# Performance work log

Measured on AMD Instinct MI355X. Metric: run time of the kernel, lower is better.

Reference implementation:

```python
import jax, jax.numpy as jnp
import numpy as np

EPS = 1e-5
DN = ('NCHW', 'OIHW', 'NCHW')

def conv(x, w, b, stride, pad):
    y = jax.lax.conv_general_dilated(x, w, (stride, stride), [(pad, pad), (pad, pad)], dimension_numbers=DN)
    return y + b[None, :, None, None]

def instance_norm(x, gamma, beta):
    # normalize over spatial dims per (N, C)
    mu = jnp.mean(x, axis=(2, 3), keepdims=True)
    var = jnp.var(x, axis=(2, 3), keepdims=True)
    xh = (x - mu) * jax.lax.rsqrt(var + EPS)
    return xh * gamma[None, :, None, None] + beta[None, :, None, None]

def lrelu(x):
    return jnp.where(x >= 0, x, 0.2 * x)

def block(x, w, b, g, be, stride, pad):
    return lrelu(instance_norm(conv(x, w, b, stride, pad), g, be))

def setup_inputs() -> dict:
    key = jax.random.key(0)
    ks = jax.random.split(key, 16)
    dim = 64
    def rn(k, shape, s=0.05):
        return jax.random.normal(k, shape, dtype=jnp.float32) * s
    inp = {
        'x':   jax.random.normal(ks[0], (256, 3, 64, 64), dtype=jnp.float32),
        'w1': rn(ks[1], (dim, 3, 5, 5)),        'b1': jnp.zeros((dim,), jnp.float32),
        'g1': jnp.ones((dim,), jnp.float32),    'be1': jnp.zeros((dim,), jnp.float32),
        'w2': rn(ks[2], (dim*2, dim, 5, 5)),    'b2': jnp.zeros((dim*2,), jnp.float32),
        'g2': jnp.ones((dim*2,), jnp.float32),  'be2': jnp.zeros((dim*2,), jnp.float32),
        'w3': rn(ks[3], (dim*4, dim*2, 5, 5)),  'b3': jnp.zeros((dim*4,), jnp.float32),
        'g3': jnp.ones((dim*4,), jnp.float32),  'be3': jnp.zeros((dim*4,), jnp.float32),
        'w4': rn(ks[4], (dim*4, dim*4, 3, 3)),  'b4': jnp.zeros((dim*4,), jnp.float32),
        'g4': jnp.ones((dim*4,), jnp.float32),  'be4': jnp.zeros((dim*4,), jnp.float32),
        # MBD tensor T: (in_features=4096, out_features=64, kernel_dims=50), init N(0,1)
        'T':  jax.random.normal(ks[5], (4096, 64, 50), dtype=jnp.float32),
        'fc_w': rn(ks[6], (1000, 4096 + 64), s=0.02),
        'fc_b': jnp.zeros((1000,), jnp.float32),
    }
    return inp

def reference(x, w1, b1, g1, be1, w2, b2, g2, be2, w3, b3, g3, be3, w4, b4, g4, be4, T, fc_w, fc_b):
    bs = x.shape[0]
    f = block(x, w1, b1, g1, be1, 2, 2)   # (bs,64,32,32)
    f = block(f, w2, b2, g2, be2, 2, 2)   # (bs,128,16,16)
    f = block(f, w3, b3, g3, be3, 2, 2)   # (bs,256,8,8)
    f = block(f, w4, b4, g4, be4, 2, 1)   # (bs,256,4,4)
    feat = f.reshape(bs, -1)              # (bs,4096)
    # minibatch discrimination
    M = jnp.einsum('bi,iok->bok', feat, T)          # (bs,64,50)
    norm = jnp.sum(jnp.abs(M[None] - M[:, None]), axis=3)  # (bs,bs,64); [i,j]=|M_i-M_j|
    o_b = jnp.sum(jnp.exp(-norm), axis=0) - 1.0     # (bs,64)
    mb = jnp.concatenate([feat, o_b], axis=1)       # (bs,4160)
    y = mb @ fc_w.T + fc_b                          # (bs,1000)
    return feat, y
```

## Files before the change

### kernel.cpp

```cpp
#include <hip/hip_runtime.h>
#include <hip/hip_fp16.h>
#include <math.h>

#define EPSF 1e-5f

typedef __attribute__((ext_vector_type(4))) float  floatx4;
typedef __attribute__((ext_vector_type(4))) short  short4v;
typedef __attribute__((ext_vector_type(8))) short  short8v;

__device__ __forceinline__ unsigned short cvt_bf16(float f){
  unsigned u = __float_as_uint(f);
  unsigned r = (u + 0x7FFFu + ((u >> 16) & 1u)) >> 16;
  return (unsigned short)r;
}
__device__ __forceinline__ float bf2f(unsigned short h){
  return __uint_as_float(((unsigned)h) << 16);
}
__device__ __forceinline__ short8v ld_frag(const unsigned short* p){
  short4v lo = *(const short4v*)p;
  short4v hi = *(const short4v*)(p + 4);
  return __builtin_shufflevector(lo, hi, 0,1,2,3,4,5,6,7);
}
__device__ __forceinline__ float lrelu(float x){ return x >= 0.f ? x : 0.2f*x; }

__global__ __launch_bounds__(256) void prep_k(const float* __restrict__ w1, const float* __restrict__ w2,
                                              const float* __restrict__ w3, const float* __restrict__ w4,
                                              unsigned short* __restrict__ wb1, unsigned short* __restrict__ wb2,
                                              unsigned short* __restrict__ wb3, unsigned short* __restrict__ wb4,
                                              float* __restrict__ SQ){
  int b = blockIdx.x, t = threadIdx.x;
  if (b < 32){
    int idx = b*256 + t;
    int j = idx&7, lane = (idx>>3)&63, ks = (idx>>9)&3, grp = idx>>11;
    int co = grp*16 + (lane&15);
    int k = ks*32 + ((lane>>4)<<3) + j;
    int tap6 = k>>2, ci = k&3;
    int kh = tap6/6, kw = tap6 - kh*6;
    float v = 0.f;
    if (ci < 3 && kh < 5 && kw < 5) v = w1[(co*3 + ci)*25 + kh*5 + kw];
    wb1[idx] = cvt_bf16(v);
  } else if (b < 832){
    int idx = (b-32)*256 + t;
    int grp = idx/25600, rem = idx - grp*25600;
    int tap = rem/1024, rem2 = rem - tap*1024;
    int ccg = rem2>>9, lane = (rem2>>3)&63, j = rem2&7;
    int co = grp*16 + (lane&15);
    int ci = ccg*32 + ((lane>>4)<<3) + j;
    wb2[idx] = cvt_bf16(w2[(co*64 + ci)*25 + tap]);
  } else if (b < 4032){
    int idx = (b-832)*256 + t;
    int grp = idx/51200, rem = idx - grp*51200;
    int tap = rem/2048, rem2 = rem - tap*2048;
    int ccg = rem2>>9, lane = (rem2>>3)&63, j = rem2&7;
    int co = grp*16 + (lane&15);
    int ci = ccg*32 + ((lane>>4)<<3) + j;
    wb3[idx] = cvt_bf16(w3[(co*128 + ci)*25 + tap]);
  } else if (b < 6336){
    int idx = (b-4032)*256 + t;
    int grp = idx/36864, rem = idx - grp*36864;
    int tap = rem/4096, rem2 = rem - tap*4096;
    int ccg = rem2>>9, lane = (rem2>>3)&63, j = rem2&7;
    int co = grp*16 + (lane&15);
    int ci = ccg*32 + ((lane>>4)<<3) + j;
    wb4[idx] = cvt_bf16(w4[(co*256 + ci)*9 + tap]);
  } else {
    int idx = (b-6336)*256 + t;
    SQ[idx] = 0.f;
  }
}

__global__ __launch_bounds__(256) void packT_k(const float* __restrict__ T,
                                               unsigned short* __restrict__ Tp){
  const int b = blockIdx.x, t = threadIdx.x;
  __shared__ float tile[32][133];
  const int nb = b % 25, kt = b / 25;
  const int n0 = nb*128, k0 = kt*32;
  #pragma unroll
  for (int m=0;m<4;m++){
    int idx = m*256 + t;
    int row = idx>>5, c4 = (idx&31)<<2;
    const float4 v = *(const float4*)&T[(k0+row)*3200 + n0 + c4];
    tile[row][c4]   = v.x; tile[row][c4+1] = v.y;
    tile[row][c4+2] = v.z; tile[row][c4+3] = v.w;
  }
  __syncthreads();
  #pragma unroll
  for (int m=0;m<2;m++){
    int c = m*256 + t;
    int ngl = c>>6, lane = c&63, q = lane>>4, r = lane&15;
    unsigned short h[8];
    #pragma unroll
    for (int j=0;j<8;j++) h[j] = cvt_bf16(tile[q*8+j][ngl*16 + r]);
    *(uint4*)&Tp[(((nb*8 + ngl)*128 + kt)*64 + lane)*8] = *(const uint4*)h;
  }
}

__global__ __launch_bounds__(256) void packW_k(const float* __restrict__ W,
                                               unsigned short* __restrict__ Wp){
  int idx = blockIdx.x*256 + threadIdx.x;
  int lane = idx & 63, rem = idx >> 6;
  int kt = rem % 130, ng = rem / 130;
  int q = lane>>4, r = lane&15;
  int orow = ng*16 + r, k = kt*32 + (q<<3);
  unsigned short h[8] = {0,0,0,0,0,0,0,0};
  if (orow < 1000){
    float4 v0 = *(const float4*)&W[orow*4160 + k];
    float4 v1 = *(const float4*)&W[orow*4160 + k + 4];
    h[0]=cvt_bf16(v0.x); h[1]=cvt_bf16(v0.y); h[2]=cvt_bf16(v0.z); h[3]=cvt_bf16(v0.w);
    h[4]=cvt_bf16(v1.x); h[5]=cvt_bf16(v1.y); h[6]=cvt_bf16(v1.z); h[7]=cvt_bf16(v1.w);
  }
  *(uint4*)&Wp[idx*8] = *(const uint4*)h;
}

__global__ __launch_bounds__(256) void conv1_k(const float* __restrict__ x, const unsigned short* __restrict__ wb1P,
                                               float* __restrict__ S1, float* __restrict__ Q1,
                                               unsigned short* __restrict__ f1raw){
  const int t = threadIdx.x, n = blockIdx.x>>1, half = blockIdx.x&1;
  const int w = t>>6, lane = t&63, q = lane>>4, l16 = lane&15;
  __shared__ __align__(16) unsigned short img[36*68*4];
  short8v bf[4][4];
  #pragma unroll
  for (int nt=0;nt<4;nt++)
    #pragma unroll
    for (int ks=0;ks<4;ks++)
      bf[nt][ks] = *(const short8v*)&wb1P[((nt*4+ks)*64 + lane)*8];
  for (int i=t; i<4896; i+=256) ((unsigned*)img)[i] = 0u;
  __syncthreads();
  for (int idx=t; idx<1680; idx+=256){
    int ci = idx/560, rem = idx - ci*560;
    int tih = rem>>4, iw4 = (rem&15)<<2;
    int ih = half*32 - 2 + tih;
    if ((unsigned)ih < 64u){
      float4 v = *(const float4*)&x[((n*3+ci)<<12) + (ih<<6) + iw4];
      int base = (tih*68 + iw4 + 2)*4 + ci;
      img[base]    = cvt_bf16(v.x);
      img[base+4]  = cvt_bf16(v.y);
      img[base+8]  = cvt_bf16(v.z);
      img[base+12] = cvt_bf16(v.w);
    }
  }
  __syncthreads();
  floatx4 acc[8][4];
  #pragma unroll
  for (int mi=0;mi<8;mi++)
    #pragma unroll
    for (int nt=0;nt<4;nt++) acc[mi][nt] = (floatx4){0.f,0.f,0.f,0.f};
  #pragma unroll
  for (int mi=0; mi<8; mi++){
    int r = w*8 + mi;
    int ohl = r>>1, ow = ((r&1)<<4) + l16;
    #pragma unroll
    for (int ks=0; ks<4; ks++){
      int t0 = ks*8 + 2*q;
      int kh = t0/6, kw = t0 - kh*6;
      short8v a = ld_frag(&img[((ohl*2+kh)*68 + ow*2 + kw)*4]);
      #pragma unroll
      for (int nt=0; nt<4; nt++)
        acc[mi][nt] = __builtin_amdgcn_mfma_f32_16x16x32_bf16(a, bf[nt][ks], acc[mi][nt], 0,0,0);
    }
  }
  float sreg[4] = {0,0,0,0}, qreg[4] = {0,0,0,0};
  #pragma unroll
  for (int mi=0;mi<8;mi++){
    int r = w*8 + mi;
    #pragma unroll
    for (int nt=0;nt<4;nt++)
      #pragma unroll
      for (int e=0;e<4;e++){
        float v = acc[mi][nt][e];
        sreg[nt] += v; qreg[nt] += v*v;
        int px = half*512 + (r<<4) + (q<<2) + e;
        f1raw[(((n<<10)+px)<<6) + (nt<<4) + l16] = cvt_bf16(v);
      }
  }
  #pragma unroll
  for (int nt=0;nt<4;nt++){
    float s = sreg[nt], qq = qreg[nt];
    s  += __shfl_xor(s,16,64);  s  += __shfl_xor(s,32,64);
    qq += __shfl_xor(qq,16,64); qq += __shfl_xor(qq,32,64);
    if (q==0){
      atomicAdd(&S1[(n<<6) + (nt<<4) + l16], s);
      atomicAdd(&Q1[(n<<6) + (nt<<4) + l16], qq);
    }
  }
}

__global__ __launch_bounds__(512) void conv2_k(const unsigned short* __restrict__ fin,
                                               const unsigned short* __restrict__ wbP,
                                               const float* __restrict__ S1, const float* __restrict__ Q1,
                                               const float* __restrict__ g1, const float* __restrict__ be1,
                                               float* __restrict__ S2, float* __restrict__ Q2,
                                               unsigned short* __restrict__ fout){
  const int t = threadIdx.x;
  const int n = blockIdx.x >> 1, half = blockIdx.x & 1;
  const int w = t>>6, lane = t&63, q = lane>>4, l16 = lane&15;
  const int rw = w&1, cw = w>>1;
  __shared__ __align__(16) unsigned short tile[684*40];
  __shared__ float gmA[64], btA[64];
  if (t < 64){
    float S = S1[(n<<6)+t], Q = Q1[(n<<6)+t];
    float mu = S*(1.f/1024.f), var = fmaxf(Q*(1.f/1024.f) - mu*mu, 0.f);
    float r = rsqrtf(var+EPSF)*g1[t];
    gmA[t] = r; btA[t] = be1[t] - mu*r;
  }
  __syncthreads();
  floatx4 acc[4][2];
  #pragma unroll
  for (int mt=0;mt<4;mt++)
    #pragma unroll
    for (int nt=0;nt<2;nt++) acc[mt][nt] = (floatx4){0.f,0.f,0.f,0.f};
  int cellb[4];
  #pragma unroll
  for (int mt=0;mt<4;mt++){
    int r = rw*64 + mt*16 + l16;
    int ohl = r>>4, ow = r&15;
    cellb[mt] = (2*ohl)*36 + 2*ow;
  }
  for (int ccg = 0; ccg < 2; ccg++){
    const int cc = ccg<<5;
    if (ccg) __syncthreads();
    #pragma unroll
    for (int it=0; it<6; it++){
      int idx = it*512 + t;
      if (idx < 2736){
        int cell = idx>>2, ci0 = (idx&3)<<3;
        int tih = cell/36, tiw = cell - tih*36;
        int ih = half*16 + tih - 2, iw = tiw - 2;
        uint4 v = {0u,0u,0u,0u};
        if ((unsigned)ih < 32u && (unsigned)iw < 32u){
          v = *(const uint4*)&fin[(((n*32+ih)*32 + iw)<<6) + cc + ci0];
          unsigned short* hp = (unsigned short*)&v;
          #pragma unroll
          for (int jj=0;jj<8;jj++){
            int c = cc + ci0 + jj;
            hp[jj] = cvt_bf16(lrelu(bf2f(hp[jj])*gmA[c]+btA[c]));
          }
        }
        *(uint4*)&tile[cell*40 + ci0] = v;
      }
    }
    __syncthreads();
    const unsigned short* bp[2];
    #pragma unroll
    for (int nt=0;nt<2;nt++)
      bp[nt] = wbP + ((((cw*2+nt)*25)*2 + ccg)<<9) + lane*8;
    short8v bq[2][4];
    #pragma unroll
    for (int p=0;p<4;p++)
      #pragma unroll
      for (int nt=0;nt<2;nt++) bq[nt][p] = *(const short8v*)(bp[nt] + (p<<10));
    #pragma unroll
    for (int tap=0; tap<25; tap++){
      const int kh = tap/5, kw = tap - kh*5;
      const int aoff = kh*36 + kw;
      short8v a[4];
      #pragma unroll
      for (int mt=0;mt<4;mt++) a[mt] = *(const short8v*)&tile[(cellb[mt]+aoff)*40 + q*8];
      #pragma unroll
      for (int mt=0;mt<4;mt++)
        #pragma unroll
        for (int nt=0;nt<2;nt++)
          acc[mt][nt] = __builtin_amdgcn_mfma_f32_16x16x32_bf16(a[mt], bq[nt][tap&3], acc[mt][nt], 0,0,0);
      if (tap+4 < 25){
        #pragma unroll
        for (int nt=0;nt<2;nt++) bq[nt][tap&3] = *(const short8v*)(bp[nt] + ((tap+4)<<10));
      }
    }
  }
  #pragma unroll
  for (int nt=0;nt<2;nt++){
    int co = cw*32 + nt*16 + l16;
    float s=0.f, qq=0.f;
    #pragma unroll
    for (int mt=0;mt<4;mt++)
      #pragma unroll
      for (int e=0;e<4;e++){ float xv = acc[mt][nt][e]; s += xv; qq += xv*xv; }
    s  += __shfl_xor(s,16,64);  s  += __shfl_xor(s,32,64);
    qq += __shfl_xor(qq,16,64); qq += __shfl_xor(qq,32,64);
    if (q == 0){
      atomicAdd(&S2[n*128 + co], s);
      atomicAdd(&Q2[n*128 + co], qq);
    }
    #pragma unroll
    for (int mt=0;mt<4;mt++)
      #pragma unroll
      for (int e=0;e<4;e++){
        int px = half*128 + rw*64 + mt*16 + q*4 + e;
        fout[((n<<8) + px)*128 + co] = cvt_bf16(acc[mt][nt][e]);
      }
  }
}

__global__ __launch_bounds__(512) void conv3_k(const unsigned short* __restrict__ fin,
                                               const unsigned short* __restrict__ wbP,
                                               const float* __restrict__ S2, const float* __restrict__ Q2,
                                               const float* __restrict__ g2, const float* __restrict__ be2,
                                               const float* __restrict__ g, const float* __restrict__ be,
                                               unsigned short* __restrict__ fout){
  const int t = threadIdx.x, n = blockIdx.x, co0 = blockIdx.y<<7;
  const int w = t>>6, lane = t&63, q = lane>>4, l16 = lane&15;
  const int rw = w&1, cw = w>>1;
  __shared__ __align__(16) unsigned short tile[361*40];
  __shared__ float gmA[128], btA[128];
  __shared__ float SQs[2][128], SQq[2][128];
  if (t < 128){
    float S = S2[n*128+t], Q = Q2[n*128+t];
    float mu = S*(1.f/256.f), var = fmaxf(Q*(1.f/256.f) - mu*mu, 0.f);
    float r = rsqrtf(var+EPSF)*g2[t];
    gmA[t] = r; btA[t] = be2[t] - mu*r;
  }
  __syncthreads();
  floatx4 acc[2][2];
  #pragma unroll
  for (int mt=0;mt<2;mt++)
    #pragma unroll
    for (int nt=0;nt<2;nt++) acc[mt][nt] = (floatx4){0.f,0.f,0.f,0.f};
  int cellb[2];
  #pragma unroll
  for (int mt=0;mt<2;mt++){
    int r = rw*32 + mt*16 + l16;
    int oh = r>>3, ow = r&7;
    cellb[mt] = (2*oh)*19 + 2*ow;
  }
  for (int ccg = 0; ccg < 4; ccg++){
    const int cc = ccg<<5;
    if (ccg) __syncthreads();
    #pragma unroll
    for (int it=0; it<3; it++){
      int idx = it*512 + t;
      if (idx < 1444){
        int cell = idx>>2, ci0 = (idx&3)<<3;
        int tih = cell/19, tiw = cell - tih*19;
        int ih = tih - 2, iw = tiw - 2;
        uint4 v = {0u,0u,0u,0u};
        if ((unsigned)ih < 16u && (unsigned)iw < 16u){
          v = *(const uint4*)&fin[(((n*16+ih)*16 + iw)<<7) + cc + ci0];
          unsigned short* hp = (unsigned short*)&v;
          #pragma unroll
          for (int jj=0;jj<8;jj++){
            int c = cc + ci0 + jj;
            hp[jj] = cvt_bf16(lrelu(bf2f(hp[jj])*gmA[c]+btA[c]));
          }
        }
        *(uint4*)&tile[cell*40 + ci0] = v;
      }
    }
    __syncthreads();
    const unsigned short* bp[2];
    #pragma unroll
    for (int nt=0;nt<2;nt++)
      bp[nt] = wbP + (((((co0>>4)+cw*2+nt)*25)*4 + ccg)<<9) + lane*8;
    short8v bq[2][4];
    #pragma unroll
    for (int p=0;p<4;p++)
      #pragma unroll
      for (int nt=0;nt<2;nt++) bq[nt][p] = *(const short8v*)(bp[nt] + (p<<11));
    #pragma unroll
    for (int tap=0; tap<25; tap++){
      const int kh = tap/5, kw = tap - kh*5;
      const int aoff = kh*19 + kw;
      short8v a[2];
      #pragma unroll
      for (int mt=0;mt<2;mt++) a[mt] = *(const short8v*)&tile[(cellb[mt]+aoff)*40 + q*8];
      #pragma unroll
      for (int mt=0;mt<2;mt++)
        #pragma unroll
        for (int nt=0;nt<2;nt++)
          acc[mt][nt] = __builtin_amdgcn_mfma_f32_16x16x32_bf16(a[mt], bq[nt][tap&3], acc[mt][nt], 0,0,0);
      if (tap+4 < 25){
        #pragma unroll
        for (int nt=0;nt<2;nt++) bq[nt][tap&3] = *(const short8v*)(bp[nt] + ((tap+4)<<11));
      }
    }
  }
  #pragma unroll
  for (int nt=0;nt<2;nt++){
    int lcol = cw*32 + nt*16 + l16;
    float s=0.f, qq=0.f;
    #pragma unroll
    for (int mt=0;mt<2;mt++)
      #pragma unroll
      for (int e=0;e<4;e++){ float xv = acc[mt][nt][e]; s += xv; qq += xv*xv; }
    s  += __shfl_xor(s,16,64);  s  += __shfl_xor(s,32,64);
    qq += __shfl_xor(qq,16,64); qq += __shfl_xor(qq,32,64);
    if (q == 0){ SQs[rw][lcol] = s; SQq[rw][lcol] = qq; }
  }
  __syncthreads();
  #pragma unroll
  for (int nt=0;nt<2;nt++){
    int lcol = cw*32 + nt*16 + l16, co = co0 + lcol;
    float S = SQs[0][lcol] + SQs[1][lcol];
    float Q = SQq[0][lcol] + SQq[1][lcol];
    float mu = S*(1.f/64.f), var = fmaxf(Q*(1.f/64.f) - mu*mu, 0.f);
    float gmv = rsqrtf(var+EPSF)*g[co];
    float btv = be[co] - mu*gmv;
    #pragma unroll
    for (int mt=0;mt<2;mt++)
      #pragma unroll
      for (int e=0;e<4;e++){
        int row = rw*32 + mt*16 + q*4 + e;
        fout[((n<<6) + row)*256 + co] = cvt_bf16(lrelu(acc[mt][nt][e]*gmv+btv));
      }
  }
}

__global__ __launch_bounds__(256) void conv4_k(const unsigned short* __restrict__ fin,
                                               const unsigned short* __restrict__ wbP,
                                               const float* __restrict__ g, const float* __restrict__ be,
                                               float* __restrict__ feat, unsigned short* __restrict__ featb){
  const int t = threadIdx.x;
  const int n0 = blockIdx.x << 1, co0 = blockIdx.y << 6;
  const int w = t>>6, lane = t&63, q = lane>>4, l16 = lane&15;
  const int rw = w&1, cw = w>>1;
  __shared__ __align__(16) unsigned short tile[2*81*40];
  floatx4 acc[2];
  acc[0] = (floatx4){0.f,0.f,0.f,0.f};
  acc[1] = (floatx4){0.f,0.f,0.f,0.f};
  const int oh = l16>>2, ow = l16&3;
  const int cellb = (2*oh)*9 + 2*ow;
  for (int ccg = 0; ccg < 8; ccg++){
    const int cc = ccg<<5;
    if (ccg) __syncthreads();
    #pragma unroll
    for (int it=0; it<3; it++){
      int idx = it*256 + t;
      if (idx < 648){
        int img = idx >= 324 ? 1 : 0;
        int rem = idx - img*324;
        int cell = rem>>2, ci0 = (rem&3)<<3;
        int tih = cell/9, tiw = cell - tih*9;
        int ih = tih - 1, iw = tiw - 1;
        uint4 v = {0u,0u,0u,0u};
        if ((unsigned)ih < 8u && (unsigned)iw < 8u)
          v = *(const uint4*)&fin[((((n0+img)*8+ih)*8 + iw)<<8) + cc + ci0];
        *(uint4*)&tile[(img*81+cell)*40 + ci0] = v;
      }
    }
    __syncthreads();
    const unsigned short* bp[2];
    #pragma unroll
    for (int nt=0;nt<2;nt++)
      bp[nt] = wbP + (((((co0>>4)+cw*2+nt)*9)*8 + ccg)<<9) + lane*8;
    short8v bq[2][4];
    #pragma unroll
    for (int p=0;p<4;p++)
      #pragma unroll
      for (int nt=0;nt<2;nt++) bq[nt][p] = *(const short8v*)(bp[nt] + (p<<12));
    #pragma unroll
    for (int tap=0; tap<9; tap++){
      const int kh = tap/3, kw = tap - kh*3;
      short8v a = *(const short8v*)&tile[(rw*81 + cellb + kh*9 + kw)*40 + q*8];
      #pragma unroll
      for (int nt=0;nt<2;nt++)
        acc[nt] = __builtin_amdgcn_mfma_f32_16x16x32_bf16(a, bq[nt][tap&3], acc[nt], 0,0,0);
      if (tap+4 < 9){
        #pragma unroll
        for (int nt=0;nt<2;nt++) bq[nt][tap&3] = *(const short8v*)(bp[nt] + ((tap+4)<<12));
      }
    }
  }
  const int nn = n0 + rw;
  #pragma unroll
  for (int nt=0;nt<2;nt++){
    int co = co0 + cw*32 + nt*16 + l16;
    float s=0.f, qq=0.f;
    #pragma unroll
    for (int e=0;e<4;e++){ float xv = acc[nt][e]; s += xv; qq += xv*xv; }
    s  += __shfl_xor(s,16,64);  s  += __shfl_xor(s,32,64);
    qq += __shfl_xor(qq,16,64); qq += __shfl_xor(qq,32,64);
    float mu = s*(1.f/16.f), var = fmaxf(qq*(1.f/16.f) - mu*mu, 0.f);
    float gmv = rsqrtf(var+EPSF)*g[co];
    float btv = be[co] - mu*gmv;
    #pragma unroll
    for (int e=0;e<4;e++){
      int px = q*4 + e;
      float vv = lrelu(acc[nt][e]*gmv+btv);
      feat [(nn<<12) + (co<<4) + px] = vv;
      featb[(nn<<12) + (co<<4) + px] = cvt_bf16(vv);
    }
  }
}

__global__ __launch_bounds__(256) void gemmM_k(const unsigned short* __restrict__ A,
                                               const unsigned short* __restrict__ Tp,
                                               float* __restrict__ Cp){
  const int t = threadIdx.x;
  const int n0 = blockIdx.x<<7, b0 = blockIdx.y<<7, k0 = blockIdx.z<<9;
  const int w = t>>6, lane = t&63, q = lane>>4, l16 = lane&15;
  const int rw = w&1, cw = w>>1;
  floatx4 acc[4][4];
  #pragma unroll
  for (int mt=0;mt<4;mt++)
    #pragma unroll
    for (int nt=0;nt<4;nt++) acc[mt][nt] = (floatx4){0.f,0.f,0.f,0.f};
  const unsigned short* Ab[4];
  const unsigned short* Bb[4];
  #pragma unroll
  for (int mt=0;mt<4;mt++)
    Ab[mt] = A + (b0 + (rw<<6) + (mt<<4) + l16)*4096 + k0 + (q<<3);
  #pragma unroll
  for (int nt=0;nt<4;nt++)
    Bb[nt] = Tp + ((((n0>>4) + (cw<<2) + nt)*128 + (k0>>5))*64 + lane)*8;
  #pragma unroll 4
  for (int kt=0; kt<16; kt++){
    short8v af[4], bfr[4];
    #pragma unroll
    for (int mt=0;mt<4;mt++) af[mt] = *(const short8v*)(Ab[mt] + kt*32);
    #pragma unroll
    for (int nt=0;nt<4;nt++) bfr[nt] = *(const short8v*)(Bb[nt] + kt*512);
    #pragma unroll
    for (int mt=0;mt<4;mt++)
      #pragma unroll
      for (int nt=0;nt<4;nt++)
        acc[mt][nt] = __builtin_amdgcn_mfma_f32_16x16x32_bf16(af[mt], bfr[nt], acc[mt][nt], 0,0,0);
  }
  float* C = Cp + blockIdx.z * 819200;
  #pragma unroll
  for (int mt=0;mt<4;mt++)
    #pragma unroll
    for (int nt=0;nt<4;nt++)
      #pragma unroll
      for (int e=0;e<4;e++){
        int row = b0 + (rw<<6) + (mt<<4) + (q<<2) + e;
        int col = n0 + (cw<<6) + (nt<<4) + l16;
        C[row*3200 + col] = acc[mt][nt][e];
      }
}

__global__ __launch_bounds__(256) void reduceM_k(const float* __restrict__ Cp, __half* __restrict__ Mh){
  int idx = blockIdx.x*256 + threadIdx.x;
  if (idx >= 851968) return;
  int i = idx / 3328, r = idx - i*3328;
  int o = r / 52, k = r - o*52;
  float v = 0.f;
  if (k < 50){
    int src = i*3200 + o*50 + k;
    #pragma unroll
    for (int s = 0; s < 8; s++) v += Cp[s*819200 + src];
  }
  Mh[idx] = __float2half(v);
}

__global__ __launch_bounds__(256) void pair_k(const __half* __restrict__ Mh,
                                              float* __restrict__ ob, unsigned short* __restrict__ obb){
  const int j = blockIdx.x, t = threadIdx.x;
  __shared__ __align__(16) __half2 Mj[1664];
  __shared__ float red[256];
  for (int k=t; k<1664; k+=256) Mj[k] = *(const __half2*)&Mh[j*3328 + (k<<1)];
  __syncthreads();
  const int o = t & 63, ss = t >> 6;
  const __half2* mjp = &Mj[o*26];
  float sum = 0.f;
  for (int i = ss<<6; i < (ss<<6)+64; i++){
    const __half2* mip = (const __half2*)&Mh[i*3328 + o*52];
    __half2 acch = __float2half2_rn(0.f);
    #pragma unroll
    for (int k2=0;k2<26;k2++){
      __half2 d = __hsub2(mip[k2], mjp[k2]);
      acch = __hadd2(acch, __habs2(d));
    }
    float dsum = __low2float(acch) + __high2float(acch);
    sum += __expf(-dsum);
  }
  red[(o<<2)+ss] = sum;
  __syncthreads();
  if (t < 64){
    float v = red[t<<2] + red[(t<<2)+1] + red[(t<<2)+2] + red[(t<<2)+3] - 1.0f;
    ob[(j<<6)+t] = v;
    obb[(j<<6)+t] = cvt_bf16(v);
  }
}

__global__ __launch_bounds__(256) void gemmFC_k(const unsigned short* __restrict__ featb,
                                                const unsigned short* __restrict__ obb,
                                                const unsigned short* __restrict__ Wp,
                                                float* __restrict__ Cp){
  const int t = threadIdx.x;
  const int o0 = blockIdx.x<<7, b0 = blockIdx.y<<7, kz = blockIdx.z;
  const int w = t>>6, lane = t&63, q = lane>>4, l16 = lane&15;
  const int rw = w&1, cw = w>>1;
  floatx4 acc[4][4];
  #pragma unroll
  for (int mt=0;mt<4;mt++)
    #pragma unroll
    for (int nt=0;nt<4;nt++) acc[mt][nt] = (floatx4){0.f,0.f,0.f,0.f};
  int rowb[4];
  #pragma unroll
  for (int mt=0;mt<4;mt++) rowb[mt] = b0 + (rw<<6) + (mt<<4) + l16;
  const unsigned short* Bb[4];
  #pragma unroll
  for (int nt=0;nt<4;nt++)
    Bb[nt] = Wp + ((((o0>>4) + (cw<<2) + nt)*130 + kz*10)*64 + lane)*8;
  #pragma unroll 2
  for (int kt=0; kt<10; kt++){
    int k = kz*320 + kt*32 + (q<<3);
    short8v af[4], bfr[4];
    #pragma unroll
    for (int mt=0;mt<4;mt++)
      af[mt] = (k < 4096) ? *(const short8v*)&featb[rowb[mt]*4096 + k]
                          : *(const short8v*)&obb[rowb[mt]*64 + (k-4096)];
    #pragma unroll
    for (int nt=0;nt<4;nt++) bfr[nt] = *(const short8v*)(Bb[nt] + kt*512);
    #pragma unroll
    for (int mt=0;mt<4;mt++)
      #pragma unroll
      for (int nt=0;nt<4;nt++)
        acc[mt][nt] = __builtin_amdgcn_mfma_f32_16x16x32_bf16(af[mt], bfr[nt], acc[mt][nt], 0,0,0);
  }
  float* C = Cp + blockIdx.z * 256000;
  #pragma unroll
  for (int mt=0;mt<4;mt++)
    #pragma unroll
    for (int nt=0;nt<4;nt++)
      #pragma unroll
      for (int e=0;e<4;e++){
        int row = b0 + (rw<<6) + (mt<<4) + (q<<2) + e;
        int col = o0 + (cw<<6) + (nt<<4) + l16;
        if (col < 1000) C[row*1000 + col] = acc[mt][nt][e];
      }
}

__global__ __launch_bounds__(256) void reduceY_k(const float* __restrict__ Cp, const float* __restrict__ bias,
                                                 float* __restrict__ y){
  int idx = blockIdx.x * 256 + threadIdx.x;
  if (idx >= 256000) return;
  int o = idx % 1000;
  float r = bias[o];
  #pragma unroll
  for (int s = 0; s < 13; s++) r += Cp[s*256000 + idx];
  y[idx] = r;
}

extern "C" void kernel_launch(void* const* d_in, const int* in_sizes, int n_in,
                              void* d_out, int out_size, void* d_ws, size_t ws_size,
                              hipStream_t stream){
  const float* x   = (const float*)d_in[0];
  const float* w1  = (const float*)d_in[1];
  const float* g1  = (const float*)d_in[3];
  const float* be1 = (const float*)d_in[4];
  const float* w2  = (const float*)d_in[5];
  const float* g2  = (const float*)d_in[7];
  const float* be2 = (const float*)d_in[8];
  const float* w3  = (const float*)d_in[9];
  const float* g3  = (const float*)d_in[11];
  const float* be3 = (const float*)d_in[12];
  const float* w4  = (const float*)d_in[13];
  const float* g4  = (const float*)d_in[15];
  const float* be4 = (const float*)d_in[16];
  const float* T   = (const float*)d_in[17];
  const float* fcw = (const float*)d_in[18];
  const float* fcb = (const float*)d_in[19];
  float* out = (float*)d_out;
  float* ws  = (float*)d_ws;

  unsigned short* f1raw = (unsigned short*)ws;
  unsigned short* Tp    = (unsigned short*)ws;
  unsigned short* f2    = (unsigned short*)(ws + 8388608);
  unsigned short* f3    = (unsigned short*)(ws + 12582912);
  unsigned short* featb = (unsigned short*)(ws + 14680064);
  unsigned short* wb1   = (unsigned short*)(ws + 15204352);
  unsigned short* wb2   = (unsigned short*)(ws + 15208448);
  unsigned short* wb3   = (unsigned short*)(ws + 15310848);
  unsigned short* wb4   = (unsigned short*)(ws + 15720448);
  float* S1    = ws + 16015360;
  float* Q1    = ws + 16031744;
  float* S2    = ws + 16048128;
  float* Q2    = ws + 16080896;
  float* Mp    = ws + 16113664;
  unsigned short* Wp  = (unsigned short*)(ws + 16113664);
  __half* Mh   = (__half*)(ws + 22667264);
  float* obuf  = ws + 23093248;
  unsigned short* obb = (unsigned short*)(ws + 23109632);
  float* yp    = ws + 23117824;
  float* feat  = out;
  float* y     = out + 1048576;

  prep_k<<<dim3(6720), 256, 0, stream>>>(w1, w2, w3, w4, wb1, wb2, wb3, wb4, S1);

  conv1_k<<<dim3(512),     256, 0, stream>>>(x, wb1, S1, Q1, f1raw);
  conv2_k<<<dim3(512),     512, 0, stream>>>(f1raw, wb2, S1, Q1, g1, be1, S2, Q2, f2);
  packT_k<<<dim3(3200),    256, 0, stream>>>(T, Tp);
  conv3_k<<<dim3(256, 2),  512, 0, stream>>>(f2, wb3, S2, Q2, g2, be2, g3, be3, f3);
  conv4_k<<<dim3(128, 4),  256, 0, stream>>>(f3, wb4, g4, be4, feat, featb);

  gemmM_k  <<<dim3(25, 2, 8),  256, 0, stream>>>(featb, Tp, Mp);
  reduceM_k<<<dim3(3328),      256, 0, stream>>>(Mp, Mh);
  packW_k  <<<dim3(2080),      256, 0, stream>>>(fcw, Wp);
  pair_k   <<<dim3(256),       256, 0, stream>>>(Mh, obuf, obb);
  gemmFC_k <<<dim3(8, 2, 13),  256, 0, stream>>>(featb, obb, Wp, yp);
  reduceY_k<<<dim3(1000),      256, 0, stream>>>(yp, fcb, y);
}
```

Before: 338.2 us.

## Swizzle conv LDS tiles and pad MBD rows for 16-byte pair loads

The conv2/conv3/conv4 LDS tiles get an XOR swizzle of the 8-channel slot index keyed on the cell index, applied on both the store and the MFMA fragment loads, to cut LDS bank conflicts. The half-precision M buffer is also padded from 52 to 56 halves per output feature, so pair_k can read with uint4 vector loads instead of half2 loads. The padding adds a little memory traffic and workspace, and the later buffers are moved to new offsets to fit.

```diff
diff --git a/kernel.cpp b/kernel.cpp
--- a/kernel.cpp
+++ b/kernel.cpp
@@ -223,7 +223,9 @@
     for (int it=0; it<6; it++){
       int idx = it*512 + t;
       if (idx < 2736){
-        int cell = idx>>2, ci0 = (idx&3)<<3;
+        int cell = idx>>2, s = idx&3;
+        int s2 = s ^ ((cell>>3)&1);
+        int ci0 = s<<3;
         int tih = cell/36, tiw = cell - tih*36;
         int ih = half*16 + tih - 2, iw = tiw - 2;
         uint4 v = {0u,0u,0u,0u};
@@ -236,7 +238,7 @@
             hp[jj] = cvt_bf16(lrelu(bf2f(hp[jj])*gmA[c]+btA[c]));
           }
         }
-        *(uint4*)&tile[cell*40 + ci0] = v;
+        *(uint4*)&tile[cell*40 + (s2<<3)] = v;
       }
     }
     __syncthreads();
@@ -255,7 +257,11 @@
       const int aoff = kh*36 + kw;
       short8v a[4];
       #pragma unroll
-      for (int mt=0;mt<4;mt++) a[mt] = *(const short8v*)&tile[(cellb[mt]+aoff)*40 + q*8];
+      for (int mt=0;mt<4;mt++){
+        int cell = cellb[mt] + aoff;
+        int q2 = q ^ ((cell>>3)&1);
+        a[mt] = *(const short8v*)&tile[cell*40 + q2*8];
+      }
       #pragma unroll
       for (int mt=0;mt<4;mt++)
         #pragma unroll
@@ -329,7 +335,9 @@
     for (int it=0; it<3; it++){
       int idx = it*512 + t;
       if (idx < 1444){
-        int cell = idx>>2, ci0 = (idx&3)<<3;
+        int cell = idx>>2, s = idx&3;
+        int s2 = s ^ ((cell>>3)&1);
+        int ci0 = s<<3;
         int tih = cell/19, tiw = cell - tih*19;
         int ih = tih - 2, iw = tiw - 2;
         uint4 v = {0u,0u,0u,0u};
@@ -342,7 +350,7 @@
             hp[jj] = cvt_bf16(lrelu(bf2f(hp[jj])*gmA[c]+btA[c]));
           }
         }
-        *(uint4*)&tile[cell*40 + ci0] = v;
+        *(uint4*)&tile[cell*40 + (s2<<3)] = v;
       }
     }
     __syncthreads();
@@ -361,7 +369,11 @@
       const int aoff = kh*19 + kw;
       short8v a[2];
       #pragma unroll
-      for (int mt=0;mt<2;mt++) a[mt] = *(const short8v*)&tile[(cellb[mt]+aoff)*40 + q*8];
+      for (int mt=0;mt<2;mt++){
+        int cell = cellb[mt] + aoff;
+        int q2 = q ^ ((cell>>3)&1);
+        a[mt] = *(const short8v*)&tile[cell*40 + q2*8];
+      }
       #pragma unroll
       for (int mt=0;mt<2;mt++)
         #pragma unroll
@@ -427,13 +439,16 @@
       if (idx < 648){
         int img = idx >= 324 ? 1 : 0;
         int rem = idx - img*324;
-        int cell = rem>>2, ci0 = (rem&3)<<3;
+        int cell = rem>>2, s = rem&3;
+        int fc = img*81 + cell;
+        int s2 = s ^ ((fc>>3)&1);
+        int ci0 = s<<3;
         int tih = cell/9, tiw = cell - tih*9;
         int ih = tih - 1, iw = tiw - 1;
         uint4 v = {0u,0u,0u,0u};
         if ((unsigned)ih < 8u && (unsigned)iw < 8u)
           v = *(const uint4*)&fin[((((n0+img)*8+ih)*8 + iw)<<8) + cc + ci0];
-        *(uint4*)&tile[(img*81+cell)*40 + ci0] = v;
+        *(uint4*)&tile[fc*40 + (s2<<3)] = v;
       }
     }
     __syncthreads();
@@ -449,7 +464,9 @@
     #pragma unroll
     for (int tap=0; tap<9; tap++){
       const int kh = tap/3, kw = tap - kh*3;
-      short8v a = *(const short8v*)&tile[(rw*81 + cellb + kh*9 + kw)*40 + q*8];
+      int fc = rw*81 + cellb + kh*9 + kw;
+      int q2 = q ^ ((fc>>3)&1);
+      short8v a = *(const short8v*)&tile[fc*40 + q2*8];
       #pragma unroll
       for (int nt=0;nt<2;nt++)
         acc[nt] = __builtin_amdgcn_mfma_f32_16x16x32_bf16(a, bq[nt][tap&3], acc[nt], 0,0,0);
@@ -529,9 +546,9 @@
 
 __global__ __launch_bounds__(256) void reduceM_k(const float* __restrict__ Cp, __half* __restrict__ Mh){
   int idx = blockIdx.x*256 + threadIdx.x;
-  if (idx >= 851968) return;
-  int i = idx / 3328, r = idx - i*3328;
-  int o = r / 52, k = r - o*52;
+  if (idx >= 917504) return;
+  int i = idx / 3584, r = idx - i*3584;
+  int o = r / 56, k = r - o*56;
   float v = 0.f;
   if (k < 50){
     int src = i*3200 + o*50 + k;
@@ -544,20 +561,24 @@
 __global__ __launch_bounds__(256) void pair_k(const __half* __restrict__ Mh,
                                               float* __restrict__ ob, unsigned short* __restrict__ obb){
   const int j = blockIdx.x, t = threadIdx.x;
-  __shared__ __align__(16) __half2 Mj[1664];
+  __shared__ __align__(16) __half2 Mj[1792];
   __shared__ float red[256];
-  for (int k=t; k<1664; k+=256) Mj[k] = *(const __half2*)&Mh[j*3328 + (k<<1)];
+  for (int k=t; k<448; k+=256) ((uint4*)Mj)[k] = ((const uint4*)&Mh[j*3584])[k];
   __syncthreads();
   const int o = t & 63, ss = t >> 6;
-  const __half2* mjp = &Mj[o*26];
+  const uint4* mjp4 = (const uint4*)&Mj[o*28];
   float sum = 0.f;
   for (int i = ss<<6; i < (ss<<6)+64; i++){
-    const __half2* mip = (const __half2*)&Mh[i*3328 + o*52];
+    const uint4* mip4 = (const uint4*)&Mh[i*3584 + o*56];
     __half2 acch = __float2half2_rn(0.f);
     #pragma unroll
-    for (int k2=0;k2<26;k2++){
-      __half2 d = __hsub2(mip[k2], mjp[k2]);
-      acch = __hadd2(acch, __habs2(d));
+    for (int u=0;u<7;u++){
+      uint4 av = mip4[u], bv = mjp4[u];
+      const __half2* ah = (const __half2*)&av;
+      const __half2* bh = (const __half2*)&bv;
+      #pragma unroll
+      for (int e=0;e<4;e++)
+        acch = __hadd2(acch, __habs2(__hsub2(ah[e], bh[e])));
     }
     float dsum = __low2float(acch) + __high2float(acch);
     sum += __expf(-dsum);
@@ -669,9 +690,9 @@
   float* Mp    = ws + 16113664;
   unsigned short* Wp  = (unsigned short*)(ws + 16113664);
   __half* Mh   = (__half*)(ws + 22667264);
-  float* obuf  = ws + 23093248;
-  unsigned short* obb = (unsigned short*)(ws + 23109632);
-  float* yp    = ws + 23117824;
+  float* obuf  = ws + 23126016;
+  unsigned short* obb = (unsigned short*)(ws + 23142400);
+  float* yp    = ws + 23150592;
   float* feat  = out;
   float* y     = out + 1048576;
 
@@ -684,7 +705,7 @@
   conv4_k<<<dim3(128, 4),  256, 0, stream>>>(f3, wb4, g4, be4, feat, featb);
 
   gemmM_k  <<<dim3(25, 2, 8),  256, 0, stream>>>(featb, Tp, Mp);
-  reduceM_k<<<dim3(3328),      256, 0, stream>>>(Mp, Mh);
+  reduceM_k<<<dim3(3584),      256, 0, stream>>>(Mp, Mh);
   packW_k  <<<dim3(2080),      256, 0, stream>>>(fcw, Wp);
   pair_k   <<<dim3(256),       256, 0, stream>>>(Mh, obuf, obb);
   gemmFC_k <<<dim3(8, 2, 13),  256, 0, stream>>>(featb, obb, Wp, yp);
```

Result: slower. 394.2 us (+16.6%).
